# Kernel optimization log

Measured on AMD Instinct MI355X. Metric: run time of the kernel, lower is better.

Reference implementation:

```python
import jax, jax.numpy as jnp
import numpy as np

VOCAB = 100000
DIM = 128
B = 16384
K = 20


def setup_inputs() -> dict:
    key = jax.random.key(0)
    k1, k2, k3, k4, k5 = jax.random.split(key, 5)
    initrange = np.sqrt(2.0 / (VOCAB + DIM)).astype(np.float32)
    return {
        "center_words": jax.random.randint(k1, (B, 1), 0, VOCAB),
        "target_words": jax.random.randint(k2, (B, 1), 0, VOCAB),
        "negative_words": jax.random.randint(k3, (B, K), 0, VOCAB),
        "V": jax.random.uniform(k4, (VOCAB, DIM), jnp.float32, -initrange, initrange),
        "U": jax.random.uniform(k5, (VOCAB, DIM), jnp.float32, -initrange, initrange),
    }


def reference(center_words, target_words, negative_words, V, U):
    # gathers: center from V table, target/negative from U table
    ce = V[center_words[:, 0]]        # [B, D]
    te = U[target_words[:, 0]]        # [B, D]
    ne = U[negative_words]            # [B, K, D]

    pos_score = jnp.sum(te * ce, axis=-1)                # [B]  (bmm [B,1,D]x[B,D,1])
    neg_scores = jnp.einsum("bkd,bd->bk", ne, ce)        # [B, K]

    pos_ls = jax.nn.log_sigmoid(pos_score)               # [B]
    neg_ls_sum = jnp.sum(jax.nn.log_sigmoid(-neg_scores), axis=1)  # [B]

    # Original torch code broadcasts [B,1] + [B] -> [B,B] then means; since
    # mean(a_i + b_j) == mean(a) + mean(b), compute the identical value
    # without materializing the BxB intermediate.
    loss = -(jnp.mean(pos_ls) + jnp.mean(neg_ls_sum))
    return loss
```

## Files before the change

kernel.cpp:

```cpp
#include <hip/hip_runtime.h>

#define B_SIZE 16384
#define K_NEG 20
#define DIM 128

__device__ __forceinline__ float logsig(float x) {
    return fminf(x, 0.0f) - __logf(1.0f + __expf(-fabsf(x)));
}

__device__ __forceinline__ float dot8(float4 a0, float4 a1, float4 b0, float4 b1) {
    return a0.x * b0.x + a0.y * b0.y + a0.z * b0.z + a0.w * b0.w
         + a1.x * b1.x + a1.y * b1.y + a1.z * b1.z + a1.w * b1.w;
}

__global__ __launch_bounds__(256) void skipgram_loss_kernel(
    const int* __restrict__ center,
    const int* __restrict__ target,
    const int* __restrict__ neg,
    const float* __restrict__ V,
    const float* __restrict__ U,
    float* __restrict__ accum)
{
    const int tid  = threadIdx.x;
    const int lane = tid & 63;
    const int wid  = tid >> 6;
    const int sub  = lane >> 4;
    const int sl   = lane & 15;

    const int e = blockIdx.x * 16 + wid * 4 + sub;

    const int c = center[e];
    const float4* vrow = (const float4*)(V + (size_t)c * DIM);
    const float4 c0 = vrow[sl * 2];
    const float4 c1 = vrow[sl * 2 + 1];

    float part[K_NEG + 1];
    {
        const int t = target[e];
        const float4* ur = (const float4*)(U + (size_t)t * DIM);
        part[0] = dot8(c0, c1, ur[sl * 2], ur[sl * 2 + 1]);
    }
    #pragma unroll
    for (int k = 0; k < K_NEG; ++k) {
        const int idx = neg[e * K_NEG + k];
        const float4* ur = (const float4*)(U + (size_t)idx * DIM);
        part[k + 1] = dot8(c0, c1, ur[sl * 2], ur[sl * 2 + 1]);
    }

    #pragma unroll
    for (int s = 1; s < 16; s <<= 1) {
        #pragma unroll
        for (int r = 0; r <= K_NEG; ++r)
            part[r] += __shfl_xor(part[r], s, 64);
    }

    float acc = logsig(part[0]);
    #pragma unroll
    for (int k = 1; k <= K_NEG; ++k)
        acc += logsig(-part[k]);

    float v = (sl == 0) ? acc : 0.0f;
    v += __shfl_xor(v, 16, 64);
    v += __shfl_xor(v, 32, 64);

    __shared__ float ssum[4];
    if (lane == 0) ssum[wid] = v;
    __syncthreads();
    if (tid == 0)
        atomicAdd(accum, ssum[0] + ssum[1] + ssum[2] + ssum[3]);
}

__global__ void finalize_kernel(const float* __restrict__ accum,
                                float* __restrict__ out)
{
    out[0] = -accum[0] * (1.0f / (float)B_SIZE);
}

extern "C" void kernel_launch(void* const* d_in, const int* in_sizes, int n_in,
                              void* d_out, int out_size, void* d_ws, size_t ws_size,
                              hipStream_t stream) {
    const int*   center = (const int*)d_in[0];
    const int*   target = (const int*)d_in[1];
    const int*   neg    = (const int*)d_in[2];
    const float* V      = (const float*)d_in[3];
    const float* U      = (const float*)d_in[4];
    float* out   = (float*)d_out;
    float* accum = (float*)d_ws;

    hipMemsetAsync(accum, 0, sizeof(float), stream);

    skipgram_loss_kernel<<<B_SIZE / 16, 256, 0, stream>>>(center, target, neg, V, U, accum);
    finalize_kernel<<<1, 1, 0, stream>>>(accum, out);
}
```

Before: 46.73 us.

## Split work into per-(example,row) dot-product tasks across 4-lane groups

Rewrites the decomposition so each 4-lane group computes one dot product between the center row and a single target or negative row, rather than a 16-lane group looping over all 21 rows. This yields 21x more independent tasks, exposes more memory-level parallelism for the random row gathers, and shortens the shuffle reduction. In exchange the center row is reloaded once per task (relying on cache), more blocks and atomics are issued, and an integer divide is needed per task.

After: 89.34 us. 91.2% more time.

```diff
diff --git a/kernel.cpp b/kernel.cpp
--- a/kernel.cpp
+++ b/kernel.cpp
@@ -3,17 +3,14 @@
 #define B_SIZE 16384
 #define K_NEG 20
 #define DIM 128
+#define NROWS 21
+#define NTASKS (B_SIZE * NROWS)
 
 __device__ __forceinline__ float logsig(float x) {
     return fminf(x, 0.0f) - __logf(1.0f + __expf(-fabsf(x)));
 }
 
-__device__ __forceinline__ float dot8(float4 a0, float4 a1, float4 b0, float4 b1) {
-    return a0.x * b0.x + a0.y * b0.y + a0.z * b0.z + a0.w * b0.w
-         + a1.x * b1.x + a1.y * b1.y + a1.z * b1.z + a1.w * b1.w;
-}
-
-__global__ __launch_bounds__(256) void skipgram_loss_kernel(
+__global__ __launch_bounds__(256, 4) void skipgram_loss_kernel(
     const int* __restrict__ center,
     const int* __restrict__ target,
     const int* __restrict__ neg,
@@ -24,47 +21,41 @@
     const int tid  = threadIdx.x;
     const int lane = tid & 63;
     const int wid  = tid >> 6;
-    const int sub  = lane >> 4;
-    const int sl   = lane & 15;
+    const int seg  = lane & 3;
+    const int task = (blockIdx.x * 4 + wid) * 16 + (lane >> 2);
 
-    const int e = blockIdx.x * 16 + wid * 4 + sub;
+    const int e = task / NROWS;
+    const int r = task - e * NROWS;
 
-    const int c = center[e];
-    const float4* vrow = (const float4*)(V + (size_t)c * DIM);
-    const float4 c0 = vrow[sl * 2];
-    const float4 c1 = vrow[sl * 2 + 1];
+    const int row = (r == 0) ? target[e] : neg[e * K_NEG + (r - 1)];
+    const int ctr = center[e];
 
-    float part[K_NEG + 1];
-    {
-        const int t = target[e];
-        const float4* ur = (const float4*)(U + (size_t)t * DIM);
-        part[0] = dot8(c0, c1, ur[sl * 2], ur[sl * 2 + 1]);
-    }
+    const float4* up = (const float4*)(U + (size_t)row * DIM) + seg * 8;
+    const float4* vp = (const float4*)(V + (size_t)ctr * DIM) + seg * 8;
+
+    float4 u[8], v[8];
     #pragma unroll
-    for (int k = 0; k < K_NEG; ++k) {
-        const int idx = neg[e * K_NEG + k];
-        const float4* ur = (const float4*)(U + (size_t)idx * DIM);
-        part[k + 1] = dot8(c0, c1, ur[sl * 2], ur[sl * 2 + 1]);
-    }
+    for (int j = 0; j < 8; ++j) u[j] = up[j];
+    #pragma unroll
+    for (int j = 0; j < 8; ++j) v[j] = vp[j];
+    __builtin_amdgcn_sched_barrier(0);
+
+    float d = 0.0f;
+    #pragma unroll
+    for (int j = 0; j < 8; ++j)
+        d += u[j].x * v[j].x + u[j].y * v[j].y + u[j].z * v[j].z + u[j].w * v[j].w;
+
+    d += __shfl_xor(d, 1, 64);
+    d += __shfl_xor(d, 2, 64);
+
+    float term = (seg == 0) ? logsig(r == 0 ? d : -d) : 0.0f;
 
     #pragma unroll
-    for (int s = 1; s < 16; s <<= 1) {
-        #pragma unroll
-        for (int r = 0; r <= K_NEG; ++r)
-            part[r] += __shfl_xor(part[r], s, 64);
-    }
-
-    float acc = logsig(part[0]);
-    #pragma unroll
-    for (int k = 1; k <= K_NEG; ++k)
-        acc += logsig(-part[k]);
-
-    float v = (sl == 0) ? acc : 0.0f;
-    v += __shfl_xor(v, 16, 64);
-    v += __shfl_xor(v, 32, 64);
+    for (int s = 4; s < 64; s <<= 1)
+        term += __shfl_xor(term, s, 64);
 
     __shared__ float ssum[4];
-    if (lane == 0) ssum[wid] = v;
+    if (lane == 0) ssum[wid] = term;
     __syncthreads();
     if (tid == 0)
         atomicAdd(accum, ssum[0] + ssum[1] + ssum[2] + ssum[3]);
@@ -89,6 +80,6 @@
 
     hipMemsetAsync(accum, 0, sizeof(float), stream);
 
-    skipgram_loss_kernel<<<B_SIZE / 16, 256, 0, stream>>>(center, target, neg, V, U, accum);
+    skipgram_loss_kernel<<<NTASKS / 64, 256, 0, stream>>>(center, target, neg, V, U, accum);
     finalize_kernel<<<1, 1, 0, stream>>>(accum, out);
 }
```
